# Optimization experiments

Hardware: AMD Instinct MI355X
Metric: run time of the kernel (lower is better)

The kernel has to match this reference:

```python
import jax, jax.numpy as jnp
import numpy as np

B, C, T = 4, 512, 4096


def setup_inputs() -> dict:
    key = jax.random.key(0)
    ks = jax.random.split(key, 9)
    s = 1.0 / np.sqrt(C)
    return {
        "x": jax.random.normal(ks[0], (B, C, T), jnp.float32),
        "Wq": jax.random.normal(ks[1], (C, C), jnp.float32) * s,
        "bq": jax.random.normal(ks[2], (C,), jnp.float32) * 0.01,
        "Wk": jax.random.normal(ks[3], (C, C), jnp.float32) * s,
        "bk": jax.random.normal(ks[4], (C,), jnp.float32) * 0.01,
        "Wv": jax.random.normal(ks[5], (C, C), jnp.float32) * s,
        "bv": jax.random.normal(ks[6], (C,), jnp.float32) * 0.01,
        "Wp": jax.random.normal(ks[7], (C, C), jnp.float32) * s,
        "bp": jax.random.normal(ks[8], (C,), jnp.float32) * 0.01,
    }


def reference(x, Wq, bq, Wk, bk, Wv, bv, Wp, bp):
    # x: [B, C, T]; kernel-size-1 causal convs == pointwise linears over channels.
    b, c, t = x.shape
    q = jnp.einsum('oc,bct->bto', Wq, x) + bq  # [B, T, C]
    k = jnp.einsum('oc,bct->bto', Wk, x) + bk
    v = jnp.einsum('oc,bct->bto', Wv, x) + bv
    scale = jnp.asarray(c, x.dtype) ** -0.5
    w = jnp.einsum('btc,bsc->bts', q, k) * scale  # [B, T, T]
    mask = jnp.tril(jnp.ones((t, t), bool))        # causal: query t attends s<=t
    w = jnp.where(mask, w, -jnp.inf)
    w = jax.nn.softmax(w, axis=-1)
    h = jnp.einsum('bts,bsc->btc', w, v)           # [B, T, C]
    out = jnp.einsum('oc,btc->bot', Wp, h) + bp[None, :, None]  # [B, C, T]
    return x + out
```

## Files before the change

kernel.cpp:

```cpp
#include <hip/hip_runtime.h>

#define NB 4
#define NC 512
#define NT 4096
#define NTILE 528

typedef __attribute__((ext_vector_type(4))) float f32x4;
typedef __attribute__((ext_vector_type(8))) short short8;

typedef const __attribute__((address_space(1))) unsigned int* gp1_t;
typedef __attribute__((address_space(3))) unsigned int* lp3_t;

__device__ __forceinline__ void gload16(const short* g, short* l) {
  __builtin_amdgcn_global_load_lds((gp1_t)g, (lp3_t)l, 16, 0, 0);
}

#define BARRIER()  asm volatile("s_barrier" ::: "memory")
#define WAITVM0()  asm volatile("s_waitcnt vmcnt(0)" ::: "memory")
#define WAITVM4()  asm volatile("s_waitcnt vmcnt(4)" ::: "memory")
#define WAITVM8()  asm volatile("s_waitcnt vmcnt(8)" ::: "memory")
#define WAITVM12() asm volatile("s_waitcnt vmcnt(12)" ::: "memory")
#define WAITVM16() asm volatile("s_waitcnt vmcnt(16)" ::: "memory")

__device__ __forceinline__ short f2bf(float f) {
  union { float f; unsigned u; } v; v.f = f;
  unsigned r = v.u + 0x7fffu + ((v.u >> 16) & 1u);
  return (short)(r >> 16);
}
__device__ __forceinline__ float bf2f(short s) {
  union { unsigned u; float f; } v; v.u = ((unsigned)(unsigned short)s) << 16;
  return v.f;
}

#define SCOL_SWZ(lane) ((((lane) & 3) ^ (((lane) >> 3) & 3)) * 8)
#define FKO_SWZ(lane)  (((((lane) >> 4) ^ (((lane) >> 1) & 3)) & 3) * 8)

template <int NBUF>
__device__ __forceinline__ void gemm_tile(const short* __restrict__ A, int lda,
                                          const short* __restrict__ Bg, int ldb,
                                          int m0, int n0, int ksteps,
                                          f32x4 (&acc)[4][4], short* lds) {
  const int tid  = threadIdx.x;
  const int lane = tid & 63;
  const int wv   = tid >> 6;
  const int wm = (wv >> 1) * 64;
  const int wn = (wv & 1) * 64;
  const int srow = wv * 16 + (lane >> 2);
  const int scol = SCOL_SWZ(lane);
  const int fm  = lane & 15;
  const int fko = FKO_SWZ(lane);

  const short* Ap0 = A  + (size_t)(m0 + srow) * lda + scol;
  const short* Ap1 = Ap0 + (size_t)64 * lda;
  const short* Bp0 = Bg + (size_t)(n0 + srow) * ldb + scol;
  const short* Bp1 = Bp0 + (size_t)64 * ldb;

  auto issue = [&](int kt) {
    short* base = lds + (kt % NBUF) * 8192;
    const int k0 = kt * 32;
    gload16(Ap0 + k0, base + wv * 512);
    gload16(Ap1 + k0, base + 2048 + wv * 512);
    gload16(Bp0 + k0, base + 4096 + wv * 512);
    gload16(Bp1 + k0, base + 6144 + wv * 512);
  };

  issue(0);
#pragma unroll
  for (int p = 1; p < NBUF - 1; ++p)
    if (p < ksteps) issue(p);

  for (int kt = 0; kt < ksteps; ++kt) {
    const short* As = lds + (kt % NBUF) * 8192;
    const short* Bs = As + 4096;
    if (kt) BARRIER();
    if constexpr (NBUF == 5) {
      if (kt + 4 < ksteps)      { issue(kt + 4); WAITVM16(); }
      else if (kt + 3 < ksteps) { WAITVM12(); }
      else if (kt + 2 < ksteps) { WAITVM8(); }
      else if (kt + 1 < ksteps) { WAITVM4(); }
      else                      { WAITVM0(); }
    } else {
      if (kt + 2 < ksteps)      { issue(kt + 2); WAITVM8(); }
      else if (kt + 1 < ksteps) { WAITVM4(); }
      else                      { WAITVM0(); }
    }
    BARRIER();
    short8 af[4], bfr[4];
#pragma unroll
    for (int i = 0; i < 4; ++i)
      af[i] = *(const short8*)(As + (wm + i * 16 + fm) * 32 + fko);
#pragma unroll
    for (int j = 0; j < 4; ++j)
      bfr[j] = *(const short8*)(Bs + (wn + j * 16 + fm) * 32 + fko);
#pragma unroll
    for (int i = 0; i < 4; ++i)
#pragma unroll
      for (int j = 0; j < 4; ++j)
        acc[i][j] = __builtin_amdgcn_mfma_f32_16x16x32_bf16(af[i], bfr[j], acc[i][j], 0, 0, 0);
  }
}

#define ACC_INIT                                  \
  f32x4 acc[4][4];                                \
  {                                               \
    const f32x4 z = {0.f, 0.f, 0.f, 0.f};         \
    for (int i = 0; i < 4; ++i)                   \
      for (int j = 0; j < 4; ++j) acc[i][j] = z;  \
  }

#define EPI_IDX                                   \
  const int lane = threadIdx.x & 63;              \
  const int wave = threadIdx.x >> 6;              \
  const int wm = (wave >> 1) * 64;                \
  const int wn = (wave & 1) * 64;

#define GEMM_LDS3 __shared__ short lds[24576];
#define GEMM_LDS5 __shared__ short lds[40960];

__device__ __forceinline__ void xcd_rowchunk(int x, int nrows, int& row, int& chunk) {
  const int xcd  = x & 7;
  const int slot = x >> 3;
  row   = nrows - 1 - (xcd + 8 * (slot >> 2));
  chunk = slot & 3;
}

__device__ __forceinline__ void pv_rowchunk(int x, int z, int& bm, int& chunk) {
  const int xcd  = x & 7;
  const int slot = x >> 3;
  int ridx = slot >> 2;
  if (z >= 2) ridx = 3 - ridx;
  bm = (ridx == 0) ? (31 - xcd)
     : (ridx == 1) ? (23 - xcd)
     : (ridx == 2) ? (8 + xcd)
                   : xcd;
  chunk = slot & 3;
}

__global__ __launch_bounds__(256) void k_transpose(const float* __restrict__ x,
                                                   short* __restrict__ xT) {
  __shared__ float tile[32][33];
  const int b  = blockIdx.z;
  const int t0 = blockIdx.x * 32;
  const int c0 = blockIdx.y * 32;
  const int tx = threadIdx.x & 31;
  const int ty = threadIdx.x >> 5;
  const float* xp = x + ((size_t)b * NC + c0) * NT + t0;
#pragma unroll
  for (int i = 0; i < 32; i += 8)
    tile[ty + i][tx] = xp[(size_t)(ty + i) * NT + tx];
  __syncthreads();
  short* op = xT + ((size_t)b * NT + t0) * NC + c0;
#pragma unroll
  for (int i = 0; i < 32; i += 8)
    op[(size_t)(ty + i) * NC + tx] = f2bf(tile[tx][ty + i]);
}

__global__ __launch_bounds__(256) void k_wcvt(const float* __restrict__ s0, const float* __restrict__ s1,
                                              const float* __restrict__ s2, const float* __restrict__ s3,
                                              short* __restrict__ d0, short* __restrict__ d1,
                                              short* __restrict__ d2, short* __restrict__ d3) {
  const float* s; short* d;
  switch (blockIdx.y) {
    case 0: s = s0; d = d0; break;
    case 1: s = s1; d = d1; break;
    case 2: s = s2; d = d2; break;
    default: s = s3; d = d3; break;
  }
  const int i = (blockIdx.x * 256 + threadIdx.x) * 4;
  const float4 v = *(const float4*)(s + i);
  short4 o;
  o.x = f2bf(v.x); o.y = f2bf(v.y); o.z = f2bf(v.z); o.w = f2bf(v.w);
  *(short4*)(d + i) = o;
}

__global__ __launch_bounds__(256, 3) void k_qkv(const short* __restrict__ xT,
                                                const short* __restrict__ Wq,
                                                const float* __restrict__ bq,
                                                const short* __restrict__ Wk,
                                                const float* __restrict__ bk,
                                                const short* __restrict__ Wv,
                                                const float* __restrict__ bv,
                                                short* __restrict__ Q,
                                                short* __restrict__ K,
                                                short* __restrict__ VT) {
  GEMM_LDS3;
  const int b = blockIdx.z;
  const int y = blockIdx.y;
  int row, chunk;
  xcd_rowchunk((int)blockIdx.x, NT / 128, row, chunk);
  const short* Xb = xT + (size_t)b * NT * NC;
  ACC_INIT;
  if (y < 2) {
    const short* W = (y == 0) ? Wq : Wk;
    const float* bias = (y == 0) ? bq : bk;
    short* O = ((y == 0) ? Q : K) + (size_t)b * NT * NC;
    const int m0 = row * 128;
    const int n0 = chunk * 128;
    gemm_tile<3>(Xb, NC, W, NC, m0, n0, NC / 32, acc, lds);
    EPI_IDX;
#pragma unroll
    for (int j = 0; j < 4; ++j) {
      const int n = n0 + wn + j * 16 + (lane & 15);
      const float bv_ = bias[n];
#pragma unroll
      for (int i = 0; i < 4; ++i) {
        const int mb = m0 + wm + i * 16 + ((lane >> 4) * 4);
#pragma unroll
        for (int r = 0; r < 4; ++r)
          O[(size_t)(mb + r) * NC + n] = f2bf(acc[i][j][r] + bv_);
      }
    }
  } else {
    const int n0 = row * 128;
    const int m0 = chunk * 128;
    gemm_tile<3>(Wv, NC, Xb, NC, m0, n0, NC / 32, acc, lds);
    EPI_IDX;
    short* O = VT + (size_t)b * NC * NT;
#pragma unroll
    for (int j = 0; j < 4; ++j) {
      const int n = n0 + wn + j * 16 + (lane & 15);
#pragma unroll
      for (int i = 0; i < 4; ++i) {
        const int mb = m0 + wm + i * 16 + ((lane >> 4) * 4);
#pragma unroll
        for (int r = 0; r < 4; ++r)
          O[(size_t)(mb + r) * NT + n] = f2bf(acc[i][j][r] + bv[mb + r]);
      }
    }
  }
}

__global__ __launch_bounds__(256, 3) void k_scores(const short* __restrict__ Q,
                                                   const short* __restrict__ K,
                                                   short* __restrict__ P,
                                                   float* __restrict__ Lrow) {
  const int p = (((int)blockIdx.x & 7) * 66) + ((int)blockIdx.x >> 3);
  int bm = 0, bn = 0;
  {
    int base = 0;
    for (int sr = 0; sr < 4; ++sr) {
      bool done = false;
      for (int sc = 0; sc <= sr; ++sc) {
        const int sz = (sc == sr) ? 36 : 64;
        if (p < base + sz) {
          const int q = p - base;
          int i, j;
          if (sc == sr) {
            i = 0;
            while ((i + 1) * (i + 2) / 2 <= q) ++i;
            j = q - i * (i + 1) / 2;
          } else { i = q >> 3; j = q & 7; }
          bm = sr * 8 + i; bn = sc * 8 + j;
          done = true; break;
        }
        base += sz;
      }
      if (done) break;
    }
  }
  GEMM_LDS3;
  const int b  = blockIdx.z;
  const int m0 = bm * 128;
  const int n0 = bn * 128;
  ACC_INIT;
  gemm_tile<3>(Q + (size_t)b * NT * NC, NC, K + (size_t)b * NT * NC, NC,
               m0, n0, NC / 32, acc, lds);
  EPI_IDX;
  const float scale = 0.04419417382415922f;
  const int idx = bm * (bm + 1) / 2 + bn;
  short* Tp = P + ((size_t)b * NTILE + (size_t)idx) * 16384;
  float* Lp = Lrow + (size_t)b * NT;
  float psum[4][4];
#pragma unroll
  for (int i = 0; i < 4; ++i)
#pragma unroll
    for (int r = 0; r < 4; ++r) psum[i][r] = 0.f;

  if (bn < bm) {
#pragma unroll
    for (int j = 0; j < 4; ++j) {
      const int ln = wn + j * 16 + (lane & 15);
#pragma unroll
      for (int i = 0; i < 4; ++i) {
        const int lmb = wm + i * 16 + ((lane >> 4) * 4);
#pragma unroll
        for (int r = 0; r < 4; ++r) {
          const short pb = f2bf(__expf(acc[i][j][r] * scale));
          Tp[(lmb + r) * 128 + ln] = pb;
          psum[i][r] += bf2f(pb);
        }
      }
    }
  } else {
#pragma unroll
    for (int j = 0; j < 4; ++j) {
      const int ln = wn + j * 16 + (lane & 15);
      const int n  = n0 + ln;
#pragma unroll
      for (int i = 0; i < 4; ++i) {
        const int lmb = wm + i * 16 + ((lane >> 4) * 4);
#pragma unroll
        for (int r = 0; r < 4; ++r) {
          const int m = m0 + lmb + r;
          float pr = 0.f;
          short pb = 0;
          if (n <= m) {
            pb = f2bf(__expf(acc[i][j][r] * scale));
            pr = bf2f(pb);
          }
          Tp[(lmb + r) * 128 + ln] = pb;
          psum[i][r] += pr;
        }
      }
    }
  }
#pragma unroll
  for (int i = 0; i < 4; ++i)
#pragma unroll
    for (int r = 0; r < 4; ++r) {
      float v = psum[i][r];
      v += __shfl_xor(v, 1);
      v += __shfl_xor(v, 2);
      v += __shfl_xor(v, 4);
      v += __shfl_xor(v, 8);
      if ((lane & 15) == 0) {
        const int m = m0 + wm + i * 16 + ((lane >> 4) * 4) + r;
        atomicAdd(&Lp[m], v);
      }
    }
}

__global__ __launch_bounds__(256, 2) void k_pv(const short* __restrict__ P,
                                               const short* __restrict__ VT,
                                               const float* __restrict__ Lr,
                                               short* __restrict__ H) {
  GEMM_LDS5;
  const int b = blockIdx.z;
  int bm, chunk;
  pv_rowchunk((int)blockIdx.x, b, bm, chunk);
  const int m0 = bm * 128;
  const int n0 = chunk * 128;
  const int ksteps = (bm + 1) * 4;

  const short* Ptri = P + ((size_t)b * NTILE + (size_t)bm * (bm + 1) / 2) * 16384;
  const short* Bg   = VT + (size_t)b * NC * NT;

  ACC_INIT;
  const int tid  = threadIdx.x;
  const int lane = tid & 63;
  const int wv   = tid >> 6;
  const int wm = (wv >> 1) * 64;
  const int wn = (wv & 1) * 64;
  const int srow = wv * 16 + (lane >> 2);
  const int scol = SCOL_SWZ(lane);
  const int fm  = lane & 15;
  const int fko = FKO_SWZ(lane);

  const short* Bp0 = Bg + (size_t)(n0 + srow) * NT + scol;
  const short* Bp1 = Bp0 + (size_t)64 * NT;

  auto issue = [&](int kt) {
    short* base = lds + (kt % 5) * 8192;
    const short* At = Ptri + (size_t)(kt >> 2) * 16384 + (kt & 3) * 32;
    const short* Ap0 = At + srow * 128 + scol;
    const int k0 = kt * 32;
    gload16(Ap0, base + wv * 512);
    gload16(Ap0 + 64 * 128, base + 2048 + wv * 512);
    gload16(Bp0 + k0, base + 4096 + wv * 512);
    gload16(Bp1 + k0, base + 6144 + wv * 512);
  };

  issue(0);
#pragma unroll
  for (int p = 1; p < 4; ++p)
    if (p < ksteps) issue(p);
  for (int kt = 0; kt < ksteps; ++kt) {
    const short* As = lds + (kt % 5) * 8192;
    const short* Bs = As + 4096;
    if (kt) BARRIER();
    if (kt + 4 < ksteps)      { issue(kt + 4); WAITVM16(); }
    else if (kt + 3 < ksteps) { WAITVM12(); }
    else if (kt + 2 < ksteps) { WAITVM8(); }
    else if (kt + 1 < ksteps) { WAITVM4(); }
    else                      { WAITVM0(); }
    BARRIER();
    short8 af[4], bfr[4];
#pragma unroll
    for (int i = 0; i < 4; ++i)
      af[i] = *(const short8*)(As + (wm + i * 16 + fm) * 32 + fko);
#pragma unroll
    for (int j = 0; j < 4; ++j)
      bfr[j] = *(const short8*)(Bs + (wn + j * 16 + fm) * 32 + fko);
#pragma unroll
    for (int i = 0; i < 4; ++i)
#pragma unroll
      for (int j = 0; j < 4; ++j)
        acc[i][j] = __builtin_amdgcn_mfma_f32_16x16x32_bf16(af[i], bfr[j], acc[i][j], 0, 0, 0);
  }

  const float* L = Lr + (size_t)b * NT;
  short* Hp = H + (size_t)b * NT * NC;
#pragma unroll
  for (int i = 0; i < 4; ++i) {
    const int mb = m0 + wm + i * 16 + ((lane >> 4) * 4);
    float rinv[4];
#pragma unroll
    for (int r = 0; r < 4; ++r) rinv[r] = 1.f / L[mb + r];
#pragma unroll
    for (int j = 0; j < 4; ++j) {
      const int n = n0 + wn + j * 16 + (lane & 15);
#pragma unroll
      for (int r = 0; r < 4; ++r)
        Hp[(size_t)(mb + r) * NC + n] = f2bf(acc[i][j][r] * rinv[r]);
    }
  }
}

__global__ __launch_bounds__(256, 2) void k_out(const short* __restrict__ W,
                                                const short* __restrict__ H,
                                                const float* __restrict__ bias,
                                                const float* __restrict__ x,
                                                float* __restrict__ out) {
  GEMM_LDS5;
  const int b = blockIdx.z;
  int row, chunk;
  xcd_rowchunk((int)blockIdx.x, NT / 128, row, chunk);
  const int n0 = row * 128;
  const int m0 = chunk * 128;
  ACC_INIT;
  gemm_tile<5>(W, NC, H + (size_t)b * NT * NC, NC, m0, n0, NC / 32, acc, lds);
  EPI_IDX;
#pragma unroll
  for (int j = 0; j < 4; ++j) {
    const int n = n0 + wn + j * 16 + (lane & 15);
#pragma unroll
    for (int i = 0; i < 4; ++i) {
      const int mb = m0 + wm + i * 16 + ((lane >> 4) * 4);
#pragma unroll
      for (int r = 0; r < 4; ++r) {
        const int m = mb + r;
        const size_t idx = ((size_t)b * NC + m) * NT + n;
        out[idx] = acc[i][j][r] + bias[m] + x[idx];
      }
    }
  }
}

extern "C" void kernel_launch(void* const* d_in, const int* in_sizes, int n_in,
                              void* d_out, int out_size, void* d_ws, size_t ws_size,
                              hipStream_t stream) {
  (void)in_sizes; (void)n_in; (void)out_size; (void)ws_size;
  const float* x  = (const float*)d_in[0];
  const float* Wq = (const float*)d_in[1];
  const float* bq = (const float*)d_in[2];
  const float* Wk = (const float*)d_in[3];
  const float* bk = (const float*)d_in[4];
  const float* Wv = (const float*)d_in[5];
  const float* bv = (const float*)d_in[6];
  const float* Wp = (const float*)d_in[7];
  const float* bp = (const float*)d_in[8];
  float* out = (float*)d_out;

  char* ws = (char*)d_ws;
  size_t off = 0;
  auto alloc = [&](size_t bytes) { char* p = ws + off; off += bytes; return p; };
  short* xT  = (short*)alloc((size_t)NB * NT * NC * 2);
  short* Qb  = (short*)alloc((size_t)NB * NT * NC * 2);
  short* Kb  = (short*)alloc((size_t)NB * NT * NC * 2);
  short* VTb = (short*)alloc((size_t)NB * NC * NT * 2);
  short* Hb  = (short*)alloc((size_t)NB * NT * NC * 2);
  short* Wqb = (short*)alloc((size_t)NC * NC * 2);
  short* Wkb = (short*)alloc((size_t)NC * NC * 2);
  short* Wvb = (short*)alloc((size_t)NC * NC * 2);
  short* Wpb = (short*)alloc((size_t)NC * NC * 2);
  float* Lr  = (float*)alloc((size_t)NB * NT * 4);
  short* Pb  = (short*)alloc((size_t)NB * NTILE * 16384 * 2);

  hipMemsetAsync(Lr, 0, (size_t)NB * NT * 4, stream);

  const dim3 blk(256);
  k_wcvt<<<dim3(NC * NC / 1024, 4), blk, 0, stream>>>(Wq, Wk, Wv, Wp, Wqb, Wkb, Wvb, Wpb);

  k_transpose<<<dim3(NT / 32, NC / 32, NB), blk, 0, stream>>>(x, xT);

  k_qkv<<<dim3(128, 3, NB), blk, 0, stream>>>(xT, Wqb, bq, Wkb, bk, Wvb, bv, Qb, Kb, VTb);

  k_scores<<<dim3(NTILE, 1, NB), blk, 0, stream>>>(Qb, Kb, Pb, Lr);
  k_pv<<<dim3(128, 1, NB), blk, 0, stream>>>(Pb, VTb, Lr, Hb);
  k_out<<<dim3(128, 1, NB), blk, 0, stream>>>(Wpb, Hb, bp, x, out);
}
```

Before: 273.2 us.

## Use double-buffered LDS for QKV/scores GEMMs, raise occupancy, use exp2 with packed bf16 cvt

Adds a two-stage LDS pipeline variant to gemm_tile and switches the QKV and scores kernels from triple to double buffering, cutting LDS per block. Launch bounds rise from 3 to 5 blocks per CU to exploit the freed LDS. The scores epilogue folds the scale into a log2e-scaled constant so it can use exp2f. Off-diagonal tiles use the hardware v_cvt_pk_bf16_f32 to pack two results per instruction. The shallower prefetch may expose more memory latency, and the tighter register budget may cause spills.

```diff
diff --git a/kernel.cpp b/kernel.cpp
--- a/kernel.cpp
+++ b/kernel.cpp
@@ -79,9 +79,12 @@
       else if (kt + 2 < ksteps) { WAITVM8(); }
       else if (kt + 1 < ksteps) { WAITVM4(); }
       else                      { WAITVM0(); }
-    } else {
+    } else if constexpr (NBUF == 3) {
       if (kt + 2 < ksteps)      { issue(kt + 2); WAITVM8(); }
       else if (kt + 1 < ksteps) { WAITVM4(); }
+      else                      { WAITVM0(); }
+    } else {
+      if (kt + 1 < ksteps)      { issue(kt + 1); WAITVM4(); }
       else                      { WAITVM0(); }
     }
     BARRIER();
@@ -114,7 +117,7 @@
   const int wm = (wave >> 1) * 64;                \
   const int wn = (wave & 1) * 64;
 
-#define GEMM_LDS3 __shared__ short lds[24576];
+#define GEMM_LDS2 __shared__ short lds[16384];
 #define GEMM_LDS5 __shared__ short lds[40960];
 
 __device__ __forceinline__ void xcd_rowchunk(int x, int nrows, int& row, int& chunk) {
@@ -173,7 +176,7 @@
   *(short4*)(d + i) = o;
 }
 
-__global__ __launch_bounds__(256, 3) void k_qkv(const short* __restrict__ xT,
+__global__ __launch_bounds__(256, 5) void k_qkv(const short* __restrict__ xT,
                                                 const short* __restrict__ Wq,
                                                 const float* __restrict__ bq,
                                                 const short* __restrict__ Wk,
@@ -183,7 +186,7 @@
                                                 short* __restrict__ Q,
                                                 short* __restrict__ K,
                                                 short* __restrict__ VT) {
-  GEMM_LDS3;
+  GEMM_LDS2;
   const int b = blockIdx.z;
   const int y = blockIdx.y;
   int row, chunk;
@@ -196,7 +199,7 @@
     short* O = ((y == 0) ? Q : K) + (size_t)b * NT * NC;
     const int m0 = row * 128;
     const int n0 = chunk * 128;
-    gemm_tile<3>(Xb, NC, W, NC, m0, n0, NC / 32, acc, lds);
+    gemm_tile<2>(Xb, NC, W, NC, m0, n0, NC / 32, acc, lds);
     EPI_IDX;
 #pragma unroll
     for (int j = 0; j < 4; ++j) {
@@ -213,7 +216,7 @@
   } else {
     const int n0 = row * 128;
     const int m0 = chunk * 128;
-    gemm_tile<3>(Wv, NC, Xb, NC, m0, n0, NC / 32, acc, lds);
+    gemm_tile<2>(Wv, NC, Xb, NC, m0, n0, NC / 32, acc, lds);
     EPI_IDX;
     short* O = VT + (size_t)b * NC * NT;
 #pragma unroll
@@ -230,7 +233,7 @@
   }
 }
 
-__global__ __launch_bounds__(256, 3) void k_scores(const short* __restrict__ Q,
+__global__ __launch_bounds__(256, 5) void k_scores(const short* __restrict__ Q,
                                                    const short* __restrict__ K,
                                                    short* __restrict__ P,
                                                    float* __restrict__ Lrow) {
@@ -258,15 +261,15 @@
       if (done) break;
     }
   }
-  GEMM_LDS3;
+  GEMM_LDS2;
   const int b  = blockIdx.z;
   const int m0 = bm * 128;
   const int n0 = bn * 128;
   ACC_INIT;
-  gemm_tile<3>(Q + (size_t)b * NT * NC, NC, K + (size_t)b * NT * NC, NC,
+  gemm_tile<2>(Q + (size_t)b * NT * NC, NC, K + (size_t)b * NT * NC, NC,
                m0, n0, NC / 32, acc, lds);
   EPI_IDX;
-  const float scale = 0.04419417382415922f;
+  const float kls = 0.06376070265f;
   const int idx = bm * (bm + 1) / 2 + bn;
   short* Tp = P + ((size_t)b * NTILE + (size_t)idx) * 16384;
   float* Lp = Lrow + (size_t)b * NT;
@@ -283,12 +286,22 @@
 #pragma unroll
       for (int i = 0; i < 4; ++i) {
         const int lmb = wm + i * 16 + ((lane >> 4) * 4);
-#pragma unroll
-        for (int r = 0; r < 4; ++r) {
-          const short pb = f2bf(__expf(acc[i][j][r] * scale));
-          Tp[(lmb + r) * 128 + ln] = pb;
-          psum[i][r] += bf2f(pb);
-        }
+        const float e0 = exp2f(acc[i][j][0] * kls);
+        const float e1 = exp2f(acc[i][j][1] * kls);
+        const float e2 = exp2f(acc[i][j][2] * kls);
+        const float e3 = exp2f(acc[i][j][3] * kls);
+        unsigned pk01, pk23;
+        asm("v_cvt_pk_bf16_f32 %0, %1, %2" : "=v"(pk01) : "v"(e0), "v"(e1));
+        asm("v_cvt_pk_bf16_f32 %0, %1, %2" : "=v"(pk23) : "v"(e2), "v"(e3));
+        Tp[(lmb + 0) * 128 + ln] = (short)(pk01 & 0xffffu);
+        Tp[(lmb + 1) * 128 + ln] = (short)(pk01 >> 16);
+        Tp[(lmb + 2) * 128 + ln] = (short)(pk23 & 0xffffu);
+        Tp[(lmb + 3) * 128 + ln] = (short)(pk23 >> 16);
+        union { unsigned u; float f; } c0, c1, c2, c3;
+        c0.u = pk01 << 16; c1.u = pk01 & 0xffff0000u;
+        c2.u = pk23 << 16; c3.u = pk23 & 0xffff0000u;
+        psum[i][0] += c0.f; psum[i][1] += c1.f;
+        psum[i][2] += c2.f; psum[i][3] += c3.f;
       }
     }
   } else {
@@ -305,7 +318,7 @@
           float pr = 0.f;
           short pb = 0;
           if (n <= m) {
-            pb = f2bf(__expf(acc[i][j][r] * scale));
+            pb = f2bf(exp2f(acc[i][j][r] * kls));
             pr = bf2f(pb);
           }
           Tp[(lmb + r) * 128 + ln] = pb;
```

Measured after the change: 407.8 us. 1.49x slower.

## Rewrite causal scores kernel with 256x256 tiles, 512 threads and pipelined LDS

Applied to the files above, without the earlier changes.

The QK^T score kernel now uses 256x256 block tiles computed by 8 waves, with double-buffered LDS staging split into A and B halves that are interleaved with MFMA phases. Each block writes up to four 128x128 probability tiles, skipping tiles above the diagonal. The exponent switches from __expf with a scale to exp2f with a pre-folded log2e scale. The aim is more operand reuse per global load and fewer blocks, at the cost of wasted work on diagonal 256 tiles and heavier register use.

```diff
diff --git a/kernel.cpp b/kernel.cpp
--- a/kernel.cpp
+++ b/kernel.cpp
@@ -21,6 +21,7 @@
 #define WAITVM8()  asm volatile("s_waitcnt vmcnt(8)" ::: "memory")
 #define WAITVM12() asm volatile("s_waitcnt vmcnt(12)" ::: "memory")
 #define WAITVM16() asm volatile("s_waitcnt vmcnt(16)" ::: "memory")
+#define WAITLGKM0() asm volatile("s_waitcnt lgkmcnt(0)" ::: "memory")
 
 __device__ __forceinline__ short f2bf(float f) {
   union { float f; unsigned u; } v; v.f = f;
@@ -230,92 +231,180 @@
   }
 }
 
-__global__ __launch_bounds__(256, 3) void k_scores(const short* __restrict__ Q,
+__global__ __launch_bounds__(512, 2) void k_scores(const short* __restrict__ Q,
                                                    const short* __restrict__ K,
                                                    short* __restrict__ P,
                                                    float* __restrict__ Lrow) {
-  const int p = (((int)blockIdx.x & 7) * 66) + ((int)blockIdx.x >> 3);
-  int bm = 0, bn = 0;
+  __shared__ short lds[65536];
+  const int x = blockIdx.x;
+  const int p = (x & 7) * 17 + (x >> 3);
+  int R = 0;
+  while ((R + 1) * (R + 2) / 2 <= p) ++R;
+  const int Cc = p - R * (R + 1) / 2;
+  const int b  = blockIdx.z;
+  const int m0 = R * 256, n0 = Cc * 256;
+
+  const int tid  = threadIdx.x;
+  const int lane = tid & 63;
+  const int wv   = tid >> 6;
+  const int wr   = wv >> 2;
+  const int wc   = wv & 3;
+  const int fm   = lane & 15;
+  const int l3   = lane >> 3;
+  const int gcg  = (lane & 7) ^ l3;
+
+  const short* Qp = Q + (size_t)b * NT * NC;
+  const short* Kp = K + (size_t)b * NT * NC;
+  const short* Asrc = Qp + (size_t)(m0 + wv * 8 + l3) * NC + gcg * 8;
+  const short* Bsrc = Kp + (size_t)(n0 + wv * 8 + l3) * NC + gcg * 8;
+
+  auto stage = [&](int c, int kt) {
+    short* dst = lds + (kt & 1) * 32768 + (c >= 4 ? 16384 : 0)
+               + (c & 3) * 4096 + wv * 512;
+    const short* src = (c < 4 ? Asrc + (size_t)(c * 64) * NC
+                              : Bsrc + (size_t)((c - 4) * 64) * NC) + kt * 64;
+    gload16(src, dst);
+  };
+
+  f32x4 acc[8][4];
   {
-    int base = 0;
-    for (int sr = 0; sr < 4; ++sr) {
-      bool done = false;
-      for (int sc = 0; sc <= sr; ++sc) {
-        const int sz = (sc == sr) ? 36 : 64;
-        if (p < base + sz) {
-          const int q = p - base;
-          int i, j;
-          if (sc == sr) {
-            i = 0;
-            while ((i + 1) * (i + 2) / 2 <= q) ++i;
-            j = q - i * (i + 1) / 2;
-          } else { i = q >> 3; j = q & 7; }
-          bm = sr * 8 + i; bn = sc * 8 + j;
-          done = true; break;
-        }
-        base += sz;
-      }
-      if (done) break;
-    }
-  }
-  GEMM_LDS3;
-  const int b  = blockIdx.z;
-  const int m0 = bm * 128;
-  const int n0 = bn * 128;
-  ACC_INIT;
-  gemm_tile<3>(Q + (size_t)b * NT * NC, NC, K + (size_t)b * NT * NC, NC,
-               m0, n0, NC / 32, acc, lds);
-  EPI_IDX;
-  const float scale = 0.04419417382415922f;
-  const int idx = bm * (bm + 1) / 2 + bn;
-  short* Tp = P + ((size_t)b * NTILE + (size_t)idx) * 16384;
+    const f32x4 z = {0.f, 0.f, 0.f, 0.f};
+    for (int i = 0; i < 8; ++i)
+      for (int j = 0; j < 4; ++j) acc[i][j] = z;
+  }
+
+  const int cg0   = ((lane >> 4) ^ (fm & 7)) * 8;
+  const int arow0 = wr * 128 + fm;
+  const int brow0 = wc * 64 + fm;
+
+  stage(0, 0); stage(1, 0); stage(2, 0); stage(3, 0);
+  stage(4, 0); stage(5, 0); stage(6, 0); stage(7, 0);
+  WAITVM0();
+  BARRIER();
+
+  for (int t = 0; t < 8; ++t) {
+    const short* Ab = lds + (t & 1) * 32768;
+    const short* Bb = Ab + 16384;
+    short8 af[8], bf0[4], bf1[4];
+#pragma unroll
+    for (int i = 0; i < 4; ++i) {
+      af[i * 2]     = *(const short8*)(Ab + (arow0 + i * 16) * 64 + cg0);
+      af[i * 2 + 1] = *(const short8*)(Ab + (arow0 + i * 16) * 64 + (cg0 ^ 32));
+    }
+#pragma unroll
+    for (int j = 0; j < 2; ++j) {
+      bf0[j * 2]     = *(const short8*)(Bb + (brow0 + j * 16) * 64 + cg0);
+      bf0[j * 2 + 1] = *(const short8*)(Bb + (brow0 + j * 16) * 64 + (cg0 ^ 32));
+    }
+    if (t < 7) { stage(0, t + 1); stage(1, t + 1); stage(2, t + 1); stage(3, t + 1); }
+    BARRIER();
+    WAITLGKM0(); __builtin_amdgcn_sched_barrier(0);
+    __builtin_amdgcn_s_setprio(1);
+#pragma unroll
+    for (int i = 0; i < 4; ++i)
+#pragma unroll
+      for (int j = 0; j < 2; ++j) {
+        acc[i][j] = __builtin_amdgcn_mfma_f32_16x16x32_bf16(af[i*2],   bf0[j*2],   acc[i][j], 0, 0, 0);
+        acc[i][j] = __builtin_amdgcn_mfma_f32_16x16x32_bf16(af[i*2+1], bf0[j*2+1], acc[i][j], 0, 0, 0);
+      }
+    __builtin_amdgcn_s_setprio(0);
+    BARRIER();
+#pragma unroll
+    for (int j = 0; j < 2; ++j) {
+      bf1[j * 2]     = *(const short8*)(Bb + (brow0 + (j + 2) * 16) * 64 + cg0);
+      bf1[j * 2 + 1] = *(const short8*)(Bb + (brow0 + (j + 2) * 16) * 64 + (cg0 ^ 32));
+    }
+    if (t < 7) { stage(4, t + 1); stage(5, t + 1); stage(6, t + 1); stage(7, t + 1); }
+    BARRIER();
+    WAITLGKM0(); __builtin_amdgcn_sched_barrier(0);
+    __builtin_amdgcn_s_setprio(1);
+#pragma unroll
+    for (int i = 0; i < 4; ++i)
+#pragma unroll
+      for (int j = 0; j < 2; ++j) {
+        acc[i][j+2] = __builtin_amdgcn_mfma_f32_16x16x32_bf16(af[i*2],   bf1[j*2],   acc[i][j+2], 0, 0, 0);
+        acc[i][j+2] = __builtin_amdgcn_mfma_f32_16x16x32_bf16(af[i*2+1], bf1[j*2+1], acc[i][j+2], 0, 0, 0);
+      }
+    __builtin_amdgcn_s_setprio(0);
+    BARRIER();
+#pragma unroll
+    for (int i = 0; i < 4; ++i) {
+      af[i * 2]     = *(const short8*)(Ab + (arow0 + (i + 4) * 16) * 64 + cg0);
+      af[i * 2 + 1] = *(const short8*)(Ab + (arow0 + (i + 4) * 16) * 64 + (cg0 ^ 32));
+    }
+    BARRIER();
+    WAITLGKM0(); __builtin_amdgcn_sched_barrier(0);
+    __builtin_amdgcn_s_setprio(1);
+#pragma unroll
+    for (int i = 0; i < 4; ++i)
+#pragma unroll
+      for (int j = 0; j < 2; ++j) {
+        acc[i+4][j+2] = __builtin_amdgcn_mfma_f32_16x16x32_bf16(af[i*2],   bf1[j*2],   acc[i+4][j+2], 0, 0, 0);
+        acc[i+4][j+2] = __builtin_amdgcn_mfma_f32_16x16x32_bf16(af[i*2+1], bf1[j*2+1], acc[i+4][j+2], 0, 0, 0);
+      }
+    __builtin_amdgcn_s_setprio(0);
+    BARRIER();
+    __builtin_amdgcn_s_setprio(1);
+#pragma unroll
+    for (int i = 0; i < 4; ++i)
+#pragma unroll
+      for (int j = 0; j < 2; ++j) {
+        acc[i+4][j] = __builtin_amdgcn_mfma_f32_16x16x32_bf16(af[i*2],   bf0[j*2],   acc[i+4][j], 0, 0, 0);
+        acc[i+4][j] = __builtin_amdgcn_mfma_f32_16x16x32_bf16(af[i*2+1], bf0[j*2+1], acc[i+4][j], 0, 0, 0);
+      }
+    __builtin_amdgcn_s_setprio(0);
+    WAITVM0();
+    BARRIER();
+  }
+
+  const float kls = 0.06376070265f;
   float* Lp = Lrow + (size_t)b * NT;
-  float psum[4][4];
-#pragma unroll
-  for (int i = 0; i < 4; ++i)
+  float psum[8][4];
+#pragma unroll
+  for (int i = 0; i < 8; ++i)
 #pragma unroll
     for (int r = 0; r < 4; ++r) psum[i][r] = 0.f;
 
-  if (bn < bm) {
+#pragma unroll
+  for (int i = 0; i < 8; ++i) {
+    const int im  = wr * 8 + i;
+    const int bmT = 2 * R + (im >> 3);
+    const int lm  = (im & 7) * 16 + ((lane >> 4) * 4);
 #pragma unroll
     for (int j = 0; j < 4; ++j) {
-      const int ln = wn + j * 16 + (lane & 15);
-#pragma unroll
-      for (int i = 0; i < 4; ++i) {
-        const int lmb = wm + i * 16 + ((lane >> 4) * 4);
+      const int jn  = wc * 4 + j;
+      const int bnT = 2 * Cc + (jn >> 3);
+      if (bnT > bmT) continue;
+      short* Tp = P + ((size_t)b * NTILE + (size_t)(bmT * (bmT + 1) / 2 + bnT)) * 16384;
+      const int ln = (jn & 7) * 16 + (lane & 15);
+      if (bnT < bmT) {
 #pragma unroll
         for (int r = 0; r < 4; ++r) {
-          const short pb = f2bf(__expf(acc[i][j][r] * scale));
-          Tp[(lmb + r) * 128 + ln] = pb;
+          const short pb = f2bf(exp2f(acc[i][j][r] * kls));
+          Tp[(lm + r) * 128 + ln] = pb;
           psum[i][r] += bf2f(pb);
         }
-      }
-    }
-  } else {
-#pragma unroll
-    for (int j = 0; j < 4; ++j) {
-      const int ln = wn + j * 16 + (lane & 15);
-      const int n  = n0 + ln;
-#pragma unroll
-      for (int i = 0; i < 4; ++i) {
-        const int lmb = wm + i * 16 + ((lane >> 4) * 4);
+      } else {
+        const int ng = bnT * 128 + ln;
+        const int mg = bmT * 128 + lm;
 #pragma unroll
         for (int r = 0; r < 4; ++r) {
-          const int m = m0 + lmb + r;
           float pr = 0.f;
           short pb = 0;
-          if (n <= m) {
-            pb = f2bf(__expf(acc[i][j][r] * scale));
+          if (ng <= mg + r) {
+            pb = f2bf(exp2f(acc[i][j][r] * kls));
             pr = bf2f(pb);
           }
-          Tp[(lmb + r) * 128 + ln] = pb;
+          Tp[(lm + r) * 128 + ln] = pb;
           psum[i][r] += pr;
         }
       }
     }
   }
 #pragma unroll
-  for (int i = 0; i < 4; ++i)
+  for (int i = 0; i < 8; ++i) {
+    const int im  = wr * 8 + i;
+    const int mg  = (2 * R + (im >> 3)) * 128 + (im & 7) * 16 + ((lane >> 4) * 4);
 #pragma unroll
     for (int r = 0; r < 4; ++r) {
       float v = psum[i][r];
@@ -323,11 +412,9 @@
       v += __shfl_xor(v, 2);
       v += __shfl_xor(v, 4);
       v += __shfl_xor(v, 8);
-      if ((lane & 15) == 0) {
-        const int m = m0 + wm + i * 16 + ((lane >> 4) * 4) + r;
-        atomicAdd(&Lp[m], v);
-      }
-    }
+      if ((lane & 15) == 0) atomicAdd(&Lp[mg + r], v);
+    }
+  }
 }
 
 __global__ __launch_bounds__(256, 2) void k_pv(const short* __restrict__ P,
@@ -485,7 +572,7 @@
 
   k_qkv<<<dim3(128, 3, NB), blk, 0, stream>>>(xT, Wqb, bq, Wkb, bk, Wvb, bv, Qb, Kb, VTb);
 
-  k_scores<<<dim3(NTILE, 1, NB), blk, 0, stream>>>(Qb, Kb, Pb, Lr);
+  k_scores<<<dim3(136, 1, NB), dim3(512), 0, stream>>>(Qb, Kb, Pb, Lr);
   k_pv<<<dim3(128, 1, NB), blk, 0, stream>>>(Pb, VTb, Lr, Hb);
   k_out<<<dim3(128, 1, NB), blk, 0, stream>>>(Wpb, Hb, bp, x, out);
 }
```

Result: slower. 331.3 us (+21.2%).
